# Performance work log

Hardware: AMD Instinct MI355X
Metric: run time of the kernel (lower is better)

The kernel has to match this reference:

```python
import jax, jax.numpy as jnp
import numpy as np

EPS = 1e-05
KEEP_RATIO = 0.7


def setup_inputs() -> dict:
    key = jax.random.key(0)
    ks = jax.random.split(key, 10)
    B, C, L, H = 8, 512, 8192, 128
    return {
        "x": jax.random.normal(ks[0], (B, C, L), dtype=jnp.float32),
        "c": jax.random.normal(ks[1], (B, C, L), dtype=jnp.float32),
        "gw1": jax.random.normal(ks[2], (H, C), dtype=jnp.float32) * 0.05,
        "gb1": jax.random.normal(ks[3], (H,), dtype=jnp.float32) * 0.05,
        "gw2": jax.random.normal(ks[4], (C, H), dtype=jnp.float32) * 0.05,
        "gb2": jax.random.normal(ks[5], (C,), dtype=jnp.float32) * 0.05,
        "mw1": jax.random.normal(ks[6], (H, C), dtype=jnp.float32) * 0.05,
        "mb1": jax.random.normal(ks[7], (H,), dtype=jnp.float32) * 0.05,
        "mw2": jax.random.normal(ks[8], (2 * C, H), dtype=jnp.float32) * 0.05,
        "mb2": jax.random.normal(ks[9], (2 * C,), dtype=jnp.float32) * 0.05,
    }


def reference(x, c, gw1, gb1, gw2, gb2, mw1, mb1, mw2, mb2):
    B, C, L = x.shape
    # per-channel stats over L
    mu_c = jnp.mean(x, axis=2, keepdims=True)                 # [B,C,1]
    var_c = jnp.var(x, axis=2, keepdims=True)                 # ddof=0
    sigma_c = jnp.sqrt(var_c + EPS)
    # per-sample stats over (C,L)
    mu_l = jnp.mean(x, axis=(1, 2), keepdims=True)            # [B,1,1]
    var_l = jnp.var(x, axis=(1, 2), keepdims=True)
    sigma_l = jnp.sqrt(var_l + EPS)
    # gate network on c (1x1 convs == channel matmuls), then mean over L
    h = jax.nn.relu(jnp.einsum('hc,bcl->bhl', gw1, c) + gb1[None, :, None])
    g = jax.nn.sigmoid(jnp.einsum('ch,bhl->bcl', gw2, h) + gb2[None, :, None])
    g_mix = jnp.mean(g, axis=2, keepdims=True)                # [B,C,1]
    mu = g_mix * mu_c + (1.0 - g_mix) * mu_l
    sigma = g_mix * sigma_c + (1.0 - g_mix) * sigma_l
    x_hat = (x - mu) / sigma
    # MLP on pooled condition -> gamma, beta
    cond_pool = jnp.mean(c, axis=2)                           # [B,C]
    hm = jax.nn.relu(jnp.einsum('hc,bc->bh', mw1, cond_pool) + mb1)
    gamma_beta = jnp.einsum('oh,bh->bo', mw2, hm) + mb2       # [B,2C]
    gamma = gamma_beta[:, :C][:, :, None]                     # [B,C,1]
    beta = gamma_beta[:, C:][:, :, None]
    y = (1.0 + gamma) * x_hat + beta
    # top-k channel mask by mean |y| over L
    imp = jnp.mean(jnp.abs(y), axis=2)                        # [B,C]
    k = max(1, int(C * KEEP_RATIO))
    _, idx = jax.lax.top_k(imp, k)                            # [B,k]
    mask = jnp.zeros((B, C), dtype=y.dtype).at[jnp.arange(B)[:, None], idx].set(1.0)
    return y * mask[:, :, None]
```

## Files before the change

kernel.cpp:

```cpp
#include <hip/hip_runtime.h>
#include <hip/hip_bf16.h>
#include <math.h>

#define NB 8
#define NC 512
#define NL 8192
#define NH 128
#define FEPS 1e-5f
#define NKEEP 358

typedef __attribute__((ext_vector_type(8))) short short8;
typedef __attribute__((ext_vector_type(4))) float f32x4;

__device__ __forceinline__ unsigned short f2bf(float x) {
  unsigned u = __float_as_uint(x);
  return (unsigned short)((u + 0x7fffu + ((u >> 16) & 1u)) >> 16);
}
__device__ __forceinline__ unsigned pack2(float a, float b) {
  return (unsigned)f2bf(a) | ((unsigned)f2bf(b) << 16);
}

__global__ __launch_bounds__(256) void k1_xstats(
    const float* __restrict__ x, float* __restrict__ xsum, float* __restrict__ xsumsq,
    const float* __restrict__ gw1, const float* __restrict__ gw2,
    unsigned short* __restrict__ gw1b, unsigned short* __restrict__ gw2b,
    float* __restrict__ csum, float* __restrict__ gsum) {
  const int bc = blockIdx.x;
  const int t = threadIdx.x;
  if (bc < 256) {
    const int i = bc * 256 + t;
    gw1b[i] = f2bf(gw1[i]);
    gw2b[i] = f2bf(gw2[i]);
    if (i < NB * NC) { csum[i] = 0.f; gsum[i] = 0.f; }
  }
  const float4* xp = reinterpret_cast<const float4*>(x + (size_t)bc * NL);
  float s1 = 0.f, s2 = 0.f;
#pragma unroll
  for (int i = 0; i < 8; ++i) {
    float4 v = xp[i * 256 + t];
    s1 += v.x + v.y + v.z + v.w;
    s2 += v.x * v.x + v.y * v.y + v.z * v.z + v.w * v.w;
  }
  for (int off = 32; off; off >>= 1) { s1 += __shfl_down(s1, off); s2 += __shfl_down(s2, off); }
  __shared__ float r1[4], r2[4];
  if ((t & 63) == 0) { r1[t >> 6] = s1; r2[t >> 6] = s2; }
  __syncthreads();
  if (t == 0) {
    xsum[bc]   = r1[0] + r1[1] + r1[2] + r1[3];
    xsumsq[bc] = r2[0] + r2[1] + r2[2] + r2[3];
  }
}

__global__ __launch_bounds__(256, 2) void k2_gate(
    const float* __restrict__ cin,
    const unsigned short* __restrict__ gw1b, const unsigned short* __restrict__ gw2b,
    const float* __restrict__ gb1, const float* __restrict__ gb2,
    float* __restrict__ gsum_g, float* __restrict__ csum_g) {
  __shared__ __align__(16) unsigned AsU[2 * 128 * 36];
  __shared__ __align__(16) unsigned short Hts[4][32][136];
  __shared__ float gsum_s[NC], csum_s[NC], gb2_s[NC];
  __shared__ float gb1_s[NH];

  const int t = threadIdx.x;
  const int lane = t & 63;
  const int w = t >> 6;
  const int r = lane & 15;
  const int kg = lane >> 4;
  const int b = blockIdx.x >> 6;
  const int l0 = (blockIdx.x & 63) * 128;

  const int p = t >> 3;
  const int q = t & 7;

  f32x4 acc0[8], acc1[8];
#pragma unroll
  for (int i = 0; i < 8; ++i) { acc0[i] = (f32x4){0.f,0.f,0.f,0.f}; acc1[i] = (f32x4){0.f,0.f,0.f,0.f}; }

  const float* cbase = cin + (size_t)b * NC * NL + l0;
  const unsigned short* gw1r = gw1b + (size_t)r * NC + kg * 8;

  f32x4 va[4], vb[4];

#define LOADA(kch) { \
    _Pragma("unroll") \
    for (int pass = 0; pass < 4; ++pass) { \
      const float* cp0 = cbase + (size_t)((kch) * 64 + 2 * p) * NL + 32 * pass + 4 * q; \
      va[pass] = __builtin_nontemporal_load(reinterpret_cast<const f32x4*>(cp0)); \
      vb[pass] = __builtin_nontemporal_load(reinterpret_cast<const f32x4*>(cp0 + NL)); \
    } }

#define WRITEA(kch, bufi) { \
    unsigned* dst = AsU + (bufi) * (128 * 36); \
    float sa = 0.f, sb = 0.f; \
    _Pragma("unroll") \
    for (int pass = 0; pass < 4; ++pass) { \
      const int ll = 32 * pass + 4 * q; \
      sa += va[pass].x + va[pass].y + va[pass].z + va[pass].w; \
      sb += vb[pass].x + vb[pass].y + vb[pass].z + vb[pass].w; \
      dst[(ll + 0) * 36 + p] = pack2(va[pass].x, vb[pass].x); \
      dst[(ll + 1) * 36 + p] = pack2(va[pass].y, vb[pass].y); \
      dst[(ll + 2) * 36 + p] = pack2(va[pass].z, vb[pass].z); \
      dst[(ll + 3) * 36 + p] = pack2(va[pass].w, vb[pass].w); \
    } \
    sa += __shfl_xor(sa, 1); sa += __shfl_xor(sa, 2); sa += __shfl_xor(sa, 4); \
    sb += __shfl_xor(sb, 1); sb += __shfl_xor(sb, 2); sb += __shfl_xor(sb, 4); \
    if ((lane & 7) == 0) { \
      atomicAdd(&csum_s[(kch) * 64 + 2 * p],     sa); \
      atomicAdd(&csum_s[(kch) * 64 + 2 * p + 1], sb); \
    } }

  LOADA(0)
  for (int i = t; i < NC; i += 256) { gsum_s[i] = 0.f; csum_s[i] = 0.f; gb2_s[i] = gb2[i]; }
  if (t < NH) gb1_s[t] = gb1[t];
  __syncthreads();
  WRITEA(0, 0)
  __syncthreads();

  for (int k = 0; k < 8; ++k) {
    const int cur = k & 1;
    if (k < 7) LOADA(k + 1)
    const unsigned* Abuf = AsU + cur * (128 * 36);
#pragma unroll
    for (int kk = 0; kk < 2; ++kk) {
      const short8 a0 = *reinterpret_cast<const short8*>(&Abuf[(32 * w + r)      * 36 + 16 * kk + 4 * kg]);
      const short8 a1 = *reinterpret_cast<const short8*>(&Abuf[(32 * w + 16 + r) * 36 + 16 * kk + 4 * kg]);
#pragma unroll
      for (int ht = 0; ht < 8; ++ht) {
        const short8 bf = *reinterpret_cast<const short8*>(
            gw1r + (size_t)(ht * 16) * NC + k * 64 + kk * 32);
        acc0[ht] = __builtin_amdgcn_mfma_f32_16x16x32_bf16(a0, bf, acc0[ht], 0, 0, 0);
        acc1[ht] = __builtin_amdgcn_mfma_f32_16x16x32_bf16(a1, bf, acc1[ht], 0, 0, 0);
      }
    }
    if (k < 7) WRITEA(k + 1, cur ^ 1)
    __syncthreads();
  }

#pragma unroll
  for (int ht = 0; ht < 8; ++ht) {
    const float bias = gb1_s[16 * ht + r];
#pragma unroll
    for (int reg = 0; reg < 4; ++reg) {
      Hts[w][4 * kg + reg][16 * ht + r]      = f2bf(fmaxf(acc0[ht][reg] + bias, 0.f));
      Hts[w][16 + 4 * kg + reg][16 * ht + r] = f2bf(fmaxf(acc1[ht][reg] + bias, 0.f));
    }
  }
  short8 af0[4], af1[4];
#pragma unroll
  for (int kk = 0; kk < 4; ++kk) {
    af0[kk] = *reinterpret_cast<const short8*>(&Hts[w][r][32 * kk + 8 * kg]);
    af1[kk] = *reinterpret_cast<const short8*>(&Hts[w][16 + r][32 * kk + 8 * kg]);
  }

  unsigned short* Bs2 = reinterpret_cast<unsigned short*>(AsU);
  const int crow = lane >> 4;
  const int bs2  = lane & 15;
  short8 bv[4];

#define LOADB2(ccn) { \
    _Pragma("unroll") \
    for (int j = 0; j < 4; ++j) { \
      const int cl = 16 * w + 4 * j + crow; \
      bv[j] = *reinterpret_cast<const short8*>(gw2b + (size_t)((ccn) * 64 + cl) * NH + bs2 * 8); \
    } }
#define WRITEB2(ccn) { \
    unsigned short* dstb = Bs2 + ((ccn) & 1) * 8192; \
    _Pragma("unroll") \
    for (int j = 0; j < 4; ++j) { \
      const int cl = 16 * w + 4 * j + crow; \
      *reinterpret_cast<short8*>(&dstb[cl * 128 + ((bs2 ^ (cl & 7)) * 8)]) = bv[j]; \
    } }

  LOADB2(0)
  WRITEB2(0)
  __syncthreads();
  for (int cc = 0; cc < 8; ++cc) {
    if (cc < 7) LOADB2(cc + 1)
    const unsigned short* Bbuf = Bs2 + (cc & 1) * 8192;
#pragma unroll
    for (int ctt = 0; ctt < 4; ++ctt) {
      f32x4 z0 = (f32x4){0.f,0.f,0.f,0.f}, z1 = (f32x4){0.f,0.f,0.f,0.f};
#pragma unroll
      for (int kk = 0; kk < 4; ++kk) {
        const short8 bf = *reinterpret_cast<const short8*>(
            &Bbuf[(16 * ctt + r) * 128 + (((4 * kk + kg) ^ (r & 7)) * 8)]);
        z0 = __builtin_amdgcn_mfma_f32_16x16x32_bf16(af0[kk], bf, z0, 0, 0, 0);
        z1 = __builtin_amdgcn_mfma_f32_16x16x32_bf16(af1[kk], bf, z1, 0, 0, 0);
      }
      const float bias = gb2_s[cc * 64 + 16 * ctt + r];
      float s = 0.f;
#pragma unroll
      for (int reg = 0; reg < 4; ++reg) {
        s += 1.f / (1.f + __expf(-(z0[reg] + bias)));
        s += 1.f / (1.f + __expf(-(z1[reg] + bias)));
      }
      s += __shfl_xor(s, 16);
      s += __shfl_xor(s, 32);
      if (lane < 16) atomicAdd(&gsum_s[cc * 64 + 16 * ctt + lane], s);
    }
    if (cc < 7) WRITEB2(cc + 1)
    __syncthreads();
  }
  for (int i = t; i < NC; i += 256) {
    atomicAdd(&gsum_g[b * NC + i], gsum_s[i]);
    atomicAdd(&csum_g[b * NC + i], csum_s[i]);
  }
}

__global__ __launch_bounds__(256) void k3_final(
    const float* __restrict__ xsum, const float* __restrict__ xsumsq,
    const float* __restrict__ csum, const float* __restrict__ gsum,
    const float* __restrict__ mw1, const float* __restrict__ mb1,
    const float* __restrict__ mw2, const float* __restrict__ mb2,
    float* __restrict__ a_arr, float* __restrict__ d_arr) {
  __shared__ __align__(16) float cp[NC];
  __shared__ __align__(16) float hm[NH];
  __shared__ float gbv[2 * NC];
  __shared__ double red[8];
  __shared__ float mu_l_s, sig_l_s;
  const int b = blockIdx.x, t = threadIdx.x;

  double s1 = 0.0, s2 = 0.0;
  for (int c = t; c < NC; c += 256) { s1 += (double)xsum[b * NC + c]; s2 += (double)xsumsq[b * NC + c]; }
  for (int off = 32; off; off >>= 1) { s1 += __shfl_down(s1, off); s2 += __shfl_down(s2, off); }
  if ((t & 63) == 0) { red[(t >> 6) * 2] = s1; red[(t >> 6) * 2 + 1] = s2; }
  for (int c = t; c < NC; c += 256) cp[c] = csum[b * NC + c] * (1.f / NL);
  __syncthreads();
  if (t == 0) {
    double S1 = red[0] + red[2] + red[4] + red[6];
    double S2 = red[1] + red[3] + red[5] + red[7];
    double n = (double)NC * NL;
    double mu = S1 / n;
    double var = S2 / n - mu * mu;
    mu_l_s = (float)mu;
    sig_l_s = (float)sqrt(var + (double)FEPS);
  }
  __syncthreads();
  if (t < NH) {
    const float4* row = reinterpret_cast<const float4*>(mw1 + (size_t)t * NC);
    const float4* cpv = reinterpret_cast<const float4*>(cp);
    float acc = mb1[t];
    for (int i = 0; i < NC / 4; ++i) {
      float4 wv = row[i], xv = cpv[i];
      acc += wv.x * xv.x + wv.y * xv.y + wv.z * xv.z + wv.w * xv.w;
    }
    hm[t] = fmaxf(acc, 0.f);
  }
  __syncthreads();
  for (int o = t; o < 2 * NC; o += 256) {
    const float4* row = reinterpret_cast<const float4*>(mw2 + (size_t)o * NH);
    const float4* hv = reinterpret_cast<const float4*>(hm);
    float acc = mb2[o];
    for (int i = 0; i < NH / 4; ++i) {
      float4 wv = row[i], xv = hv[i];
      acc += wv.x * xv.x + wv.y * xv.y + wv.z * xv.z + wv.w * xv.w;
    }
    gbv[o] = acc;
  }
  __syncthreads();
  const float mu_l = mu_l_s, sig_l = sig_l_s;
  for (int c = t; c < NC; c += 256) {
    float gm = gsum[b * NC + c] * (1.f / NL);
    double mu_c = (double)xsum[b * NC + c] / NL;
    double var_c = (double)xsumsq[b * NC + c] / NL - mu_c * mu_c;
    float sig_c = (float)sqrt(var_c + (double)FEPS);
    float mu = gm * (float)mu_c + (1.f - gm) * mu_l;
    float sg = gm * sig_c + (1.f - gm) * sig_l;
    float gamma = gbv[c], beta = gbv[NC + c];
    float A = (1.f + gamma) / sg;
    a_arr[b * NC + c] = A;
    d_arr[b * NC + c] = beta - A * mu;
  }
}

__global__ __launch_bounds__(256) void k4_y(
    const float* __restrict__ x, const float* __restrict__ a_arr,
    const float* __restrict__ d_arr, float* __restrict__ out, float* __restrict__ imp) {
  const int bc = blockIdx.x, t = threadIdx.x;
  const float A = a_arr[bc], D = d_arr[bc];
  const f32x4* xp = reinterpret_cast<const f32x4*>(x + (size_t)bc * NL);
  f32x4* op = reinterpret_cast<f32x4*>(out + (size_t)bc * NL);
  float s = 0.f;
#pragma unroll
  for (int i = 0; i < 8; ++i) {
    f32x4 v = __builtin_nontemporal_load(xp + i * 256 + t);
    f32x4 y;
    y.x = fmaf(A, v.x, D); y.y = fmaf(A, v.y, D);
    y.z = fmaf(A, v.z, D); y.w = fmaf(A, v.w, D);
    s += fabsf(y.x) + fabsf(y.y) + fabsf(y.z) + fabsf(y.w);
    __builtin_nontemporal_store(y, op + i * 256 + t);
  }
  for (int off = 32; off; off >>= 1) s += __shfl_down(s, off);
  __shared__ float rs[4];
  if ((t & 63) == 0) rs[t >> 6] = s;
  __syncthreads();
  if (t == 0) imp[bc] = rs[0] + rs[1] + rs[2] + rs[3];
}

__global__ __launch_bounds__(256) void k5_apply(
    const float* __restrict__ imp, float* __restrict__ out) {
  const int bc = blockIdx.x;
  const int b = bc >> 9;
  const int c = bc & (NC - 1);
  const int t = threadIdx.x;
  const float* row = imp + b * NC;
  const float mine = row[c];
  int cnt = 0;
#pragma unroll
  for (int jj = 0; jj < 2; ++jj) {
    const int j = jj * 256 + t;
    const float o = row[j];
    cnt += (o > mine) || (o == mine && j < c);
  }
  for (int off = 32; off; off >>= 1) cnt += __shfl_down(cnt, off);
  __shared__ int rs[4];
  if ((t & 63) == 0) rs[t >> 6] = cnt;
  __syncthreads();
  const int rank = rs[0] + rs[1] + rs[2] + rs[3];
  if (rank < NKEEP) return;
  f32x4* op = reinterpret_cast<f32x4*>(out + (size_t)bc * NL);
  const f32x4 z = (f32x4){0.f, 0.f, 0.f, 0.f};
#pragma unroll
  for (int i = 0; i < 8; ++i) __builtin_nontemporal_store(z, op + i * 256 + t);
}

extern "C" void kernel_launch(void* const* d_in, const int* in_sizes, int n_in,
                              void* d_out, int out_size, void* d_ws, size_t ws_size,
                              hipStream_t stream) {
  const float* x   = (const float*)d_in[0];
  const float* c   = (const float*)d_in[1];
  const float* gw1 = (const float*)d_in[2];
  const float* gb1 = (const float*)d_in[3];
  const float* gw2 = (const float*)d_in[4];
  const float* gb2 = (const float*)d_in[5];
  const float* mw1 = (const float*)d_in[6];
  const float* mb1 = (const float*)d_in[7];
  const float* mw2 = (const float*)d_in[8];
  const float* mb2 = (const float*)d_in[9];
  float* out = (float*)d_out;
  char* ws = (char*)d_ws;

  unsigned short* gw1b = (unsigned short*)(ws);
  unsigned short* gw2b = (unsigned short*)(ws + 131072);
  float* xsum   = (float*)(ws + 262144);
  float* xsumsq = (float*)(ws + 278528);
  float* csum   = (float*)(ws + 294912);
  float* gsum   = (float*)(ws + 311296);
  float* a_arr  = (float*)(ws + 327680);
  float* d_arr  = (float*)(ws + 344064);
  float* imp    = (float*)(ws + 360448);

  k1_xstats<<<NB * NC, 256, 0, stream>>>(x, xsum, xsumsq, gw1, gw2, gw1b, gw2b, csum, gsum);
  k2_gate<<<NB * (NL / 128), 256, 0, stream>>>(c, gw1b, gw2b, gb1, gb2, gsum, csum);
  k3_final<<<NB, 256, 0, stream>>>(xsum, xsumsq, csum, gsum, mw1, mb1, mw2, mb2, a_arr, d_arr);
  k4_y<<<NB * NC, 256, 0, stream>>>(x, a_arr, d_arr, out, imp);
  k5_apply<<<NB * NC, 256, 0, stream>>>(imp, out);
}
```

Baseline: 175.9 us.

## Fuse x statistics into gate kernel and double its block size to 512 threads

The per-channel sum and sum-of-squares reduction over x moves out of its own launch and into the gate GEMM kernel, where each wave streams one x row alongside the c tiles. Weight conversion and zeroing now run in a small separate prep kernel. The gate kernel goes from 256 to 512 threads, each wave owning 16 L-rows instead of 32, and per-channel c sums are written directly instead of through shared atomics. The aim is to overlap the x read with the c-side matrix work and drop a full-grid launch, at the cost of more memory traffic inside the gate kernel and more register and occupancy pressure.

```diff
diff --git a/kernel.cpp b/kernel.cpp
--- a/kernel.cpp
+++ b/kernel.cpp
@@ -20,44 +20,24 @@
   return (unsigned)f2bf(a) | ((unsigned)f2bf(b) << 16);
 }
 
-__global__ __launch_bounds__(256) void k1_xstats(
-    const float* __restrict__ x, float* __restrict__ xsum, float* __restrict__ xsumsq,
+__global__ __launch_bounds__(256) void k0_prep(
     const float* __restrict__ gw1, const float* __restrict__ gw2,
     unsigned short* __restrict__ gw1b, unsigned short* __restrict__ gw2b,
     float* __restrict__ csum, float* __restrict__ gsum) {
-  const int bc = blockIdx.x;
-  const int t = threadIdx.x;
-  if (bc < 256) {
-    const int i = bc * 256 + t;
-    gw1b[i] = f2bf(gw1[i]);
-    gw2b[i] = f2bf(gw2[i]);
-    if (i < NB * NC) { csum[i] = 0.f; gsum[i] = 0.f; }
-  }
-  const float4* xp = reinterpret_cast<const float4*>(x + (size_t)bc * NL);
-  float s1 = 0.f, s2 = 0.f;
-#pragma unroll
-  for (int i = 0; i < 8; ++i) {
-    float4 v = xp[i * 256 + t];
-    s1 += v.x + v.y + v.z + v.w;
-    s2 += v.x * v.x + v.y * v.y + v.z * v.z + v.w * v.w;
-  }
-  for (int off = 32; off; off >>= 1) { s1 += __shfl_down(s1, off); s2 += __shfl_down(s2, off); }
-  __shared__ float r1[4], r2[4];
-  if ((t & 63) == 0) { r1[t >> 6] = s1; r2[t >> 6] = s2; }
-  __syncthreads();
-  if (t == 0) {
-    xsum[bc]   = r1[0] + r1[1] + r1[2] + r1[3];
-    xsumsq[bc] = r2[0] + r2[1] + r2[2] + r2[3];
-  }
-}
-
-__global__ __launch_bounds__(256, 2) void k2_gate(
-    const float* __restrict__ cin,
+  int i = blockIdx.x * 256 + threadIdx.x;
+  gw1b[i] = f2bf(gw1[i]);
+  gw2b[i] = f2bf(gw2[i]);
+  if (i < NB * NC) { csum[i] = 0.f; gsum[i] = 0.f; }
+}
+
+__global__ __launch_bounds__(512, 4) void k2_gate(
+    const float* __restrict__ cin, const float* __restrict__ x,
     const unsigned short* __restrict__ gw1b, const unsigned short* __restrict__ gw2b,
     const float* __restrict__ gb1, const float* __restrict__ gb2,
-    float* __restrict__ gsum_g, float* __restrict__ csum_g) {
+    float* __restrict__ gsum_g, float* __restrict__ csum_g,
+    float* __restrict__ xsum, float* __restrict__ xsumsq) {
   __shared__ __align__(16) unsigned AsU[2 * 128 * 36];
-  __shared__ __align__(16) unsigned short Hts[4][32][136];
+  __shared__ __align__(16) unsigned short Hts[8][16][136];
   __shared__ float gsum_s[NC], csum_s[NC], gb2_s[NC];
   __shared__ float gb1_s[NH];
 
@@ -67,24 +47,28 @@
   const int r = lane & 15;
   const int kg = lane >> 4;
   const int b = blockIdx.x >> 6;
-  const int l0 = (blockIdx.x & 63) * 128;
-
-  const int p = t >> 3;
-  const int q = t & 7;
-
-  f32x4 acc0[8], acc1[8];
-#pragma unroll
-  for (int i = 0; i < 8; ++i) { acc0[i] = (f32x4){0.f,0.f,0.f,0.f}; acc1[i] = (f32x4){0.f,0.f,0.f,0.f}; }
+  const int lt = blockIdx.x & 63;
+  const int l0 = lt * 128;
+
+  const int p = t >> 4;
+  const int q = t & 15;
+
+  f32x4 acc[8];
+#pragma unroll
+  for (int i = 0; i < 8; ++i) acc[i] = (f32x4){0.f,0.f,0.f,0.f};
 
   const float* cbase = cin + (size_t)b * NC * NL + l0;
   const unsigned short* gw1r = gw1b + (size_t)r * NC + kg * 8;
 
-  f32x4 va[4], vb[4];
+  const f32x4* xp4 = reinterpret_cast<const f32x4*>(x + ((size_t)b * NC + lt * 8 + w) * NL);
+  float xs1 = 0.f, xs2 = 0.f;
+
+  f32x4 va[2], vb[2];
 
 #define LOADA(kch) { \
     _Pragma("unroll") \
-    for (int pass = 0; pass < 4; ++pass) { \
-      const float* cp0 = cbase + (size_t)((kch) * 64 + 2 * p) * NL + 32 * pass + 4 * q; \
+    for (int pass = 0; pass < 2; ++pass) { \
+      const float* cp0 = cbase + (size_t)((kch) * 64 + 2 * p) * NL + 64 * pass + 4 * q; \
       va[pass] = __builtin_nontemporal_load(reinterpret_cast<const f32x4*>(cp0)); \
       vb[pass] = __builtin_nontemporal_load(reinterpret_cast<const f32x4*>(cp0 + NL)); \
     } }
@@ -93,8 +77,8 @@
     unsigned* dst = AsU + (bufi) * (128 * 36); \
     float sa = 0.f, sb = 0.f; \
     _Pragma("unroll") \
-    for (int pass = 0; pass < 4; ++pass) { \
-      const int ll = 32 * pass + 4 * q; \
+    for (int pass = 0; pass < 2; ++pass) { \
+      const int ll = 64 * pass + 4 * q; \
       sa += va[pass].x + va[pass].y + va[pass].z + va[pass].w; \
       sb += vb[pass].x + vb[pass].y + vb[pass].z + vb[pass].w; \
       dst[(ll + 0) * 36 + p] = pack2(va[pass].x, vb[pass].x); \
@@ -102,15 +86,25 @@
       dst[(ll + 2) * 36 + p] = pack2(va[pass].z, vb[pass].z); \
       dst[(ll + 3) * 36 + p] = pack2(va[pass].w, vb[pass].w); \
     } \
-    sa += __shfl_xor(sa, 1); sa += __shfl_xor(sa, 2); sa += __shfl_xor(sa, 4); \
-    sb += __shfl_xor(sb, 1); sb += __shfl_xor(sb, 2); sb += __shfl_xor(sb, 4); \
-    if ((lane & 7) == 0) { \
-      atomicAdd(&csum_s[(kch) * 64 + 2 * p],     sa); \
-      atomicAdd(&csum_s[(kch) * 64 + 2 * p + 1], sb); \
+    sa += __shfl_xor(sa, 1); sa += __shfl_xor(sa, 2); \
+    sa += __shfl_xor(sa, 4); sa += __shfl_xor(sa, 8); \
+    sb += __shfl_xor(sb, 1); sb += __shfl_xor(sb, 2); \
+    sb += __shfl_xor(sb, 4); sb += __shfl_xor(sb, 8); \
+    if ((lane & 15) == 0) { \
+      csum_s[(kch) * 64 + 2 * p]     = sa; \
+      csum_s[(kch) * 64 + 2 * p + 1] = sb; \
+    } }
+
+#define XCHUNK(kch) { \
+    _Pragma("unroll") \
+    for (int j = 0; j < 4; ++j) { \
+      f32x4 v = xp4[lane + 64 * (4 * (kch) + j)]; \
+      xs1 += v.x + v.y + v.z + v.w; \
+      xs2 += v.x * v.x + v.y * v.y + v.z * v.z + v.w * v.w; \
     } }
 
   LOADA(0)
-  for (int i = t; i < NC; i += 256) { gsum_s[i] = 0.f; csum_s[i] = 0.f; gb2_s[i] = gb2[i]; }
+  for (int i = t; i < NC; i += 512) { gsum_s[i] = 0.f; gb2_s[i] = gb2[i]; }
   if (t < NH) gb1_s[t] = gb1[t];
   __syncthreads();
   WRITEA(0, 0)
@@ -119,55 +113,56 @@
   for (int k = 0; k < 8; ++k) {
     const int cur = k & 1;
     if (k < 7) LOADA(k + 1)
+    XCHUNK(k)
     const unsigned* Abuf = AsU + cur * (128 * 36);
 #pragma unroll
     for (int kk = 0; kk < 2; ++kk) {
-      const short8 a0 = *reinterpret_cast<const short8*>(&Abuf[(32 * w + r)      * 36 + 16 * kk + 4 * kg]);
-      const short8 a1 = *reinterpret_cast<const short8*>(&Abuf[(32 * w + 16 + r) * 36 + 16 * kk + 4 * kg]);
+      const short8 a = *reinterpret_cast<const short8*>(&Abuf[(16 * w + r) * 36 + 16 * kk + 4 * kg]);
 #pragma unroll
       for (int ht = 0; ht < 8; ++ht) {
         const short8 bf = *reinterpret_cast<const short8*>(
             gw1r + (size_t)(ht * 16) * NC + k * 64 + kk * 32);
-        acc0[ht] = __builtin_amdgcn_mfma_f32_16x16x32_bf16(a0, bf, acc0[ht], 0, 0, 0);
-        acc1[ht] = __builtin_amdgcn_mfma_f32_16x16x32_bf16(a1, bf, acc1[ht], 0, 0, 0);
+        acc[ht] = __builtin_amdgcn_mfma_f32_16x16x32_bf16(a, bf, acc[ht], 0, 0, 0);
       }
     }
     if (k < 7) WRITEA(k + 1, cur ^ 1)
     __syncthreads();
   }
 
+  for (int off = 32; off; off >>= 1) { xs1 += __shfl_down(xs1, off); xs2 += __shfl_down(xs2, off); }
+  if (lane == 0) {
+    xsum[b * NC + lt * 8 + w]   = xs1;
+    xsumsq[b * NC + lt * 8 + w] = xs2;
+  }
+
 #pragma unroll
   for (int ht = 0; ht < 8; ++ht) {
     const float bias = gb1_s[16 * ht + r];
 #pragma unroll
-    for (int reg = 0; reg < 4; ++reg) {
-      Hts[w][4 * kg + reg][16 * ht + r]      = f2bf(fmaxf(acc0[ht][reg] + bias, 0.f));
-      Hts[w][16 + 4 * kg + reg][16 * ht + r] = f2bf(fmaxf(acc1[ht][reg] + bias, 0.f));
-    }
-  }
-  short8 af0[4], af1[4];
-#pragma unroll
-  for (int kk = 0; kk < 4; ++kk) {
-    af0[kk] = *reinterpret_cast<const short8*>(&Hts[w][r][32 * kk + 8 * kg]);
-    af1[kk] = *reinterpret_cast<const short8*>(&Hts[w][16 + r][32 * kk + 8 * kg]);
-  }
+    for (int reg = 0; reg < 4; ++reg)
+      Hts[w][4 * kg + reg][16 * ht + r] = f2bf(fmaxf(acc[ht][reg] + bias, 0.f));
+  }
+  short8 af[4];
+#pragma unroll
+  for (int kk = 0; kk < 4; ++kk)
+    af[kk] = *reinterpret_cast<const short8*>(&Hts[w][r][32 * kk + 8 * kg]);
 
   unsigned short* Bs2 = reinterpret_cast<unsigned short*>(AsU);
   const int crow = lane >> 4;
   const int bs2  = lane & 15;
-  short8 bv[4];
+  short8 bv[2];
 
 #define LOADB2(ccn) { \
     _Pragma("unroll") \
-    for (int j = 0; j < 4; ++j) { \
-      const int cl = 16 * w + 4 * j + crow; \
+    for (int j = 0; j < 2; ++j) { \
+      const int cl = 8 * w + 4 * j + crow; \
       bv[j] = *reinterpret_cast<const short8*>(gw2b + (size_t)((ccn) * 64 + cl) * NH + bs2 * 8); \
     } }
 #define WRITEB2(ccn) { \
     unsigned short* dstb = Bs2 + ((ccn) & 1) * 8192; \
     _Pragma("unroll") \
-    for (int j = 0; j < 4; ++j) { \
-      const int cl = 16 * w + 4 * j + crow; \
+    for (int j = 0; j < 2; ++j) { \
+      const int cl = 8 * w + 4 * j + crow; \
       *reinterpret_cast<short8*>(&dstb[cl * 128 + ((bs2 ^ (cl & 7)) * 8)]) = bv[j]; \
     } }
 
@@ -179,21 +174,18 @@
     const unsigned short* Bbuf = Bs2 + (cc & 1) * 8192;
 #pragma unroll
     for (int ctt = 0; ctt < 4; ++ctt) {
-      f32x4 z0 = (f32x4){0.f,0.f,0.f,0.f}, z1 = (f32x4){0.f,0.f,0.f,0.f};
+      f32x4 z = (f32x4){0.f,0.f,0.f,0.f};
 #pragma unroll
       for (int kk = 0; kk < 4; ++kk) {
         const short8 bf = *reinterpret_cast<const short8*>(
             &Bbuf[(16 * ctt + r) * 128 + (((4 * kk + kg) ^ (r & 7)) * 8)]);
-        z0 = __builtin_amdgcn_mfma_f32_16x16x32_bf16(af0[kk], bf, z0, 0, 0, 0);
-        z1 = __builtin_amdgcn_mfma_f32_16x16x32_bf16(af1[kk], bf, z1, 0, 0, 0);
+        z = __builtin_amdgcn_mfma_f32_16x16x32_bf16(af[kk], bf, z, 0, 0, 0);
       }
       const float bias = gb2_s[cc * 64 + 16 * ctt + r];
       float s = 0.f;
 #pragma unroll
-      for (int reg = 0; reg < 4; ++reg) {
-        s += 1.f / (1.f + __expf(-(z0[reg] + bias)));
-        s += 1.f / (1.f + __expf(-(z1[reg] + bias)));
-      }
+      for (int reg = 0; reg < 4; ++reg)
+        s += 1.f / (1.f + __expf(-(z[reg] + bias)));
       s += __shfl_xor(s, 16);
       s += __shfl_xor(s, 32);
       if (lane < 16) atomicAdd(&gsum_s[cc * 64 + 16 * ctt + lane], s);
@@ -201,7 +193,7 @@
     if (cc < 7) WRITEB2(cc + 1)
     __syncthreads();
   }
-  for (int i = t; i < NC; i += 256) {
+  for (int i = t; i < NC; i += 512) {
     atomicAdd(&gsum_g[b * NC + i], gsum_s[i]);
     atomicAdd(&csum_g[b * NC + i], csum_s[i]);
   }
@@ -350,8 +342,8 @@
   float* d_arr  = (float*)(ws + 344064);
   float* imp    = (float*)(ws + 360448);
 
-  k1_xstats<<<NB * NC, 256, 0, stream>>>(x, xsum, xsumsq, gw1, gw2, gw1b, gw2b, csum, gsum);
-  k2_gate<<<NB * (NL / 128), 256, 0, stream>>>(c, gw1b, gw2b, gb1, gb2, gsum, csum);
+  k0_prep<<<256, 256, 0, stream>>>(gw1, gw2, gw1b, gw2b, csum, gsum);
+  k2_gate<<<NB * (NL / 128), 512, 0, stream>>>(c, x, gw1b, gw2b, gb1, gb2, gsum, csum, xsum, xsumsq);
   k3_final<<<NB, 256, 0, stream>>>(xsum, xsumsq, csum, gsum, mw1, mb1, mw2, mb2, a_arr, d_arr);
   k4_y<<<NB * NC, 256, 0, stream>>>(x, a_arr, d_arr, out, imp);
   k5_apply<<<NB * NC, 256, 0, stream>>>(imp, out);
```

After: 195.1 us. 1.11x slower.

## Halve gate-kernel L tile, raise occupancy, read gw2 fragments directly from global

Applied to the files above, without the earlier changes.

The gate kernel now processes 64 positions per block instead of 128, doubling the grid and halving accumulators, LDS and register use so four blocks can fit per CU. The gw2 LDS double-buffer staging and its per-chunk barriers are removed, and B fragments are loaded straight from global/L2. gw1 fragments are prefetched into registers before the A-tile loads, with sched barriers to control ordering. Per-block weight traffic roughly doubles because each block reloads gw1/gw2 for half the work, and global atomics also double.

```diff
diff --git a/kernel.cpp b/kernel.cpp
--- a/kernel.cpp
+++ b/kernel.cpp
@@ -51,13 +51,12 @@
   }
 }
 
-__global__ __launch_bounds__(256, 2) void k2_gate(
+__global__ __launch_bounds__(256, 4) void k2_gate(
     const float* __restrict__ cin,
     const unsigned short* __restrict__ gw1b, const unsigned short* __restrict__ gw2b,
     const float* __restrict__ gb1, const float* __restrict__ gb2,
     float* __restrict__ gsum_g, float* __restrict__ csum_g) {
-  __shared__ __align__(16) unsigned AsU[2 * 128 * 36];
-  __shared__ __align__(16) unsigned short Hts[4][32][136];
+  __shared__ __align__(16) unsigned AsU[2 * 64 * 36];
   __shared__ float gsum_s[NC], csum_s[NC], gb2_s[NC];
   __shared__ float gb1_s[NH];
 
@@ -66,34 +65,34 @@
   const int w = t >> 6;
   const int r = lane & 15;
   const int kg = lane >> 4;
-  const int b = blockIdx.x >> 6;
-  const int l0 = (blockIdx.x & 63) * 128;
+  const int b = blockIdx.x >> 7;
+  const int l0 = (blockIdx.x & 127) * 64;
 
   const int p = t >> 3;
   const int q = t & 7;
 
-  f32x4 acc0[8], acc1[8];
-#pragma unroll
-  for (int i = 0; i < 8; ++i) { acc0[i] = (f32x4){0.f,0.f,0.f,0.f}; acc1[i] = (f32x4){0.f,0.f,0.f,0.f}; }
+  f32x4 acc[8];
+#pragma unroll
+  for (int i = 0; i < 8; ++i) acc[i] = (f32x4){0.f,0.f,0.f,0.f};
 
   const float* cbase = cin + (size_t)b * NC * NL + l0;
   const unsigned short* gw1r = gw1b + (size_t)r * NC + kg * 8;
 
-  f32x4 va[4], vb[4];
+  f32x4 va[2], vb[2];
 
 #define LOADA(kch) { \
     _Pragma("unroll") \
-    for (int pass = 0; pass < 4; ++pass) { \
+    for (int pass = 0; pass < 2; ++pass) { \
       const float* cp0 = cbase + (size_t)((kch) * 64 + 2 * p) * NL + 32 * pass + 4 * q; \
       va[pass] = __builtin_nontemporal_load(reinterpret_cast<const f32x4*>(cp0)); \
       vb[pass] = __builtin_nontemporal_load(reinterpret_cast<const f32x4*>(cp0 + NL)); \
     } }
 
 #define WRITEA(kch, bufi) { \
-    unsigned* dst = AsU + (bufi) * (128 * 36); \
+    unsigned* dst = AsU + (bufi) * (64 * 36); \
     float sa = 0.f, sb = 0.f; \
     _Pragma("unroll") \
-    for (int pass = 0; pass < 4; ++pass) { \
+    for (int pass = 0; pass < 2; ++pass) { \
       const int ll = 32 * pass + 4 * q; \
       sa += va[pass].x + va[pass].y + va[pass].z + va[pass].w; \
       sb += vb[pass].x + vb[pass].y + vb[pass].z + vb[pass].w; \
@@ -105,102 +104,74 @@
     sa += __shfl_xor(sa, 1); sa += __shfl_xor(sa, 2); sa += __shfl_xor(sa, 4); \
     sb += __shfl_xor(sb, 1); sb += __shfl_xor(sb, 2); sb += __shfl_xor(sb, 4); \
     if ((lane & 7) == 0) { \
-      atomicAdd(&csum_s[(kch) * 64 + 2 * p],     sa); \
-      atomicAdd(&csum_s[(kch) * 64 + 2 * p + 1], sb); \
+      csum_s[(kch) * 64 + 2 * p]     = sa; \
+      csum_s[(kch) * 64 + 2 * p + 1] = sb; \
     } }
 
   LOADA(0)
-  for (int i = t; i < NC; i += 256) { gsum_s[i] = 0.f; csum_s[i] = 0.f; gb2_s[i] = gb2[i]; }
+  for (int i = t; i < NC; i += 256) { gsum_s[i] = 0.f; gb2_s[i] = gb2[i]; }
   if (t < NH) gb1_s[t] = gb1[t];
   __syncthreads();
   WRITEA(0, 0)
   __syncthreads();
 
   for (int k = 0; k < 8; ++k) {
-    const int cur = k & 1;
+    short8 bfr[16];
+#pragma unroll
+    for (int ht = 0; ht < 8; ++ht) {
+      bfr[2 * ht]     = *reinterpret_cast<const short8*>(gw1r + (size_t)(ht * 16) * NC + k * 64);
+      bfr[2 * ht + 1] = *reinterpret_cast<const short8*>(gw1r + (size_t)(ht * 16) * NC + k * 64 + 32);
+    }
+    __builtin_amdgcn_sched_barrier(0);
     if (k < 7) LOADA(k + 1)
-    const unsigned* Abuf = AsU + cur * (128 * 36);
+    __builtin_amdgcn_sched_barrier(0);
+    const unsigned* Abuf = AsU + (k & 1) * (64 * 36);
 #pragma unroll
     for (int kk = 0; kk < 2; ++kk) {
-      const short8 a0 = *reinterpret_cast<const short8*>(&Abuf[(32 * w + r)      * 36 + 16 * kk + 4 * kg]);
-      const short8 a1 = *reinterpret_cast<const short8*>(&Abuf[(32 * w + 16 + r) * 36 + 16 * kk + 4 * kg]);
-#pragma unroll
-      for (int ht = 0; ht < 8; ++ht) {
-        const short8 bf = *reinterpret_cast<const short8*>(
-            gw1r + (size_t)(ht * 16) * NC + k * 64 + kk * 32);
-        acc0[ht] = __builtin_amdgcn_mfma_f32_16x16x32_bf16(a0, bf, acc0[ht], 0, 0, 0);
-        acc1[ht] = __builtin_amdgcn_mfma_f32_16x16x32_bf16(a1, bf, acc1[ht], 0, 0, 0);
-      }
-    }
-    if (k < 7) WRITEA(k + 1, cur ^ 1)
+      const short8 a = *reinterpret_cast<const short8*>(&Abuf[(16 * w + r) * 36 + 16 * kk + 4 * kg]);
+#pragma unroll
+      for (int ht = 0; ht < 8; ++ht)
+        acc[ht] = __builtin_amdgcn_mfma_f32_16x16x32_bf16(a, bfr[2 * ht + kk], acc[ht], 0, 0, 0);
+    }
+    if (k < 7) WRITEA(k + 1, (k + 1) & 1)
     __syncthreads();
   }
 
+  unsigned short (*Hts)[16][136] = reinterpret_cast<unsigned short (*)[16][136]>(AsU);
 #pragma unroll
   for (int ht = 0; ht < 8; ++ht) {
     const float bias = gb1_s[16 * ht + r];
 #pragma unroll
-    for (int reg = 0; reg < 4; ++reg) {
-      Hts[w][4 * kg + reg][16 * ht + r]      = f2bf(fmaxf(acc0[ht][reg] + bias, 0.f));
-      Hts[w][16 + 4 * kg + reg][16 * ht + r] = f2bf(fmaxf(acc1[ht][reg] + bias, 0.f));
-    }
-  }
-  short8 af0[4], af1[4];
-#pragma unroll
-  for (int kk = 0; kk < 4; ++kk) {
-    af0[kk] = *reinterpret_cast<const short8*>(&Hts[w][r][32 * kk + 8 * kg]);
-    af1[kk] = *reinterpret_cast<const short8*>(&Hts[w][16 + r][32 * kk + 8 * kg]);
-  }
-
-  unsigned short* Bs2 = reinterpret_cast<unsigned short*>(AsU);
-  const int crow = lane >> 4;
-  const int bs2  = lane & 15;
-  short8 bv[4];
-
-#define LOADB2(ccn) { \
-    _Pragma("unroll") \
-    for (int j = 0; j < 4; ++j) { \
-      const int cl = 16 * w + 4 * j + crow; \
-      bv[j] = *reinterpret_cast<const short8*>(gw2b + (size_t)((ccn) * 64 + cl) * NH + bs2 * 8); \
-    } }
-#define WRITEB2(ccn) { \
-    unsigned short* dstb = Bs2 + ((ccn) & 1) * 8192; \
-    _Pragma("unroll") \
-    for (int j = 0; j < 4; ++j) { \
-      const int cl = 16 * w + 4 * j + crow; \
-      *reinterpret_cast<short8*>(&dstb[cl * 128 + ((bs2 ^ (cl & 7)) * 8)]) = bv[j]; \
-    } }
-
-  LOADB2(0)
-  WRITEB2(0)
-  __syncthreads();
+    for (int reg = 0; reg < 4; ++reg)
+      Hts[w][4 * kg + reg][16 * ht + r] = f2bf(fmaxf(acc[ht][reg] + bias, 0.f));
+  }
+  short8 af[4];
+#pragma unroll
+  for (int kk = 0; kk < 4; ++kk)
+    af[kk] = *reinterpret_cast<const short8*>(&Hts[w][r][32 * kk + 8 * kg]);
+
+  const unsigned short* gw2r = gw2b + (size_t)r * NH + kg * 8;
   for (int cc = 0; cc < 8; ++cc) {
-    if (cc < 7) LOADB2(cc + 1)
-    const unsigned short* Bbuf = Bs2 + (cc & 1) * 8192;
 #pragma unroll
     for (int ctt = 0; ctt < 4; ++ctt) {
-      f32x4 z0 = (f32x4){0.f,0.f,0.f,0.f}, z1 = (f32x4){0.f,0.f,0.f,0.f};
+      f32x4 z = (f32x4){0.f,0.f,0.f,0.f};
 #pragma unroll
       for (int kk = 0; kk < 4; ++kk) {
         const short8 bf = *reinterpret_cast<const short8*>(
-            &Bbuf[(16 * ctt + r) * 128 + (((4 * kk + kg) ^ (r & 7)) * 8)]);
-        z0 = __builtin_amdgcn_mfma_f32_16x16x32_bf16(af0[kk], bf, z0, 0, 0, 0);
-        z1 = __builtin_amdgcn_mfma_f32_16x16x32_bf16(af1[kk], bf, z1, 0, 0, 0);
+            gw2r + (size_t)(cc * 64 + 16 * ctt) * NH + kk * 32);
+        z = __builtin_amdgcn_mfma_f32_16x16x32_bf16(af[kk], bf, z, 0, 0, 0);
       }
       const float bias = gb2_s[cc * 64 + 16 * ctt + r];
       float s = 0.f;
 #pragma unroll
-      for (int reg = 0; reg < 4; ++reg) {
-        s += 1.f / (1.f + __expf(-(z0[reg] + bias)));
-        s += 1.f / (1.f + __expf(-(z1[reg] + bias)));
-      }
+      for (int reg = 0; reg < 4; ++reg)
+        s += 1.f / (1.f + __expf(-(z[reg] + bias)));
       s += __shfl_xor(s, 16);
       s += __shfl_xor(s, 32);
       if (lane < 16) atomicAdd(&gsum_s[cc * 64 + 16 * ctt + lane], s);
     }
-    if (cc < 7) WRITEB2(cc + 1)
-    __syncthreads();
-  }
+  }
+  __syncthreads();
   for (int i = t; i < NC; i += 256) {
     atomicAdd(&gsum_g[b * NC + i], gsum_s[i]);
     atomicAdd(&csum_g[b * NC + i], csum_s[i]);
@@ -351,7 +322,7 @@
   float* imp    = (float*)(ws + 360448);
 
   k1_xstats<<<NB * NC, 256, 0, stream>>>(x, xsum, xsumsq, gw1, gw2, gw1b, gw2b, csum, gsum);
-  k2_gate<<<NB * (NL / 128), 256, 0, stream>>>(c, gw1b, gw2b, gb1, gb2, gsum, csum);
+  k2_gate<<<NB * (NL / 64), 256, 0, stream>>>(c, gw1b, gw2b, gb1, gb2, gsum, csum);
   k3_final<<<NB, 256, 0, stream>>>(xsum, xsumsq, csum, gsum, mw1, mb1, mw2, mb2, a_arr, d_arr);
   k4_y<<<NB * NC, 256, 0, stream>>>(x, a_arr, d_arr, out, imp);
   k5_apply<<<NB * NC, 256, 0, stream>>>(imp, out);
```

Measured after the change: 234.4 us. 33.3% more time.

## Fuse per-channel x statistics into the gate GEMM kernel

Applied to the files above, without the earlier changes.

The standalone x-statistics pass is removed and folded into the gate kernel. Each of the 512 gate blocks now also streams 8 rows of x and reduces their sum and sum of squares, interleaving those loads with the GEMM main loop. A small prep kernel keeps the weight conversion and zeroing. The aim is to overlap the memory-bound x read with the compute-bound gate GEMM and save a launch, at the cost of more register pressure and memory traffic inside the gate kernel.

```diff
diff --git a/kernel.cpp b/kernel.cpp
--- a/kernel.cpp
+++ b/kernel.cpp
@@ -20,42 +20,22 @@
   return (unsigned)f2bf(a) | ((unsigned)f2bf(b) << 16);
 }
 
-__global__ __launch_bounds__(256) void k1_xstats(
-    const float* __restrict__ x, float* __restrict__ xsum, float* __restrict__ xsumsq,
+__global__ __launch_bounds__(256) void k0_prep(
     const float* __restrict__ gw1, const float* __restrict__ gw2,
     unsigned short* __restrict__ gw1b, unsigned short* __restrict__ gw2b,
     float* __restrict__ csum, float* __restrict__ gsum) {
-  const int bc = blockIdx.x;
-  const int t = threadIdx.x;
-  if (bc < 256) {
-    const int i = bc * 256 + t;
-    gw1b[i] = f2bf(gw1[i]);
-    gw2b[i] = f2bf(gw2[i]);
-    if (i < NB * NC) { csum[i] = 0.f; gsum[i] = 0.f; }
-  }
-  const float4* xp = reinterpret_cast<const float4*>(x + (size_t)bc * NL);
-  float s1 = 0.f, s2 = 0.f;
-#pragma unroll
-  for (int i = 0; i < 8; ++i) {
-    float4 v = xp[i * 256 + t];
-    s1 += v.x + v.y + v.z + v.w;
-    s2 += v.x * v.x + v.y * v.y + v.z * v.z + v.w * v.w;
-  }
-  for (int off = 32; off; off >>= 1) { s1 += __shfl_down(s1, off); s2 += __shfl_down(s2, off); }
-  __shared__ float r1[4], r2[4];
-  if ((t & 63) == 0) { r1[t >> 6] = s1; r2[t >> 6] = s2; }
-  __syncthreads();
-  if (t == 0) {
-    xsum[bc]   = r1[0] + r1[1] + r1[2] + r1[3];
-    xsumsq[bc] = r2[0] + r2[1] + r2[2] + r2[3];
-  }
+  int i = blockIdx.x * 256 + threadIdx.x;
+  gw1b[i] = f2bf(gw1[i]);
+  gw2b[i] = f2bf(gw2[i]);
+  if (i < NB * NC) { csum[i] = 0.f; gsum[i] = 0.f; }
 }
 
 __global__ __launch_bounds__(256, 2) void k2_gate(
-    const float* __restrict__ cin,
+    const float* __restrict__ cin, const float* __restrict__ x,
     const unsigned short* __restrict__ gw1b, const unsigned short* __restrict__ gw2b,
     const float* __restrict__ gb1, const float* __restrict__ gb2,
-    float* __restrict__ gsum_g, float* __restrict__ csum_g) {
+    float* __restrict__ gsum_g, float* __restrict__ csum_g,
+    float* __restrict__ xsum, float* __restrict__ xsumsq) {
   __shared__ __align__(16) unsigned AsU[2 * 128 * 36];
   __shared__ __align__(16) unsigned short Hts[4][32][136];
   __shared__ float gsum_s[NC], csum_s[NC], gb2_s[NC];
@@ -78,6 +58,12 @@
 
   const float* cbase = cin + (size_t)b * NC * NL + l0;
   const unsigned short* gw1r = gw1b + (size_t)r * NC + kg * 8;
+
+  const int xr = t >> 5;
+  const int xq = t & 31;
+  const float* xrow = x + ((size_t)blockIdx.x * 8 + xr) * NL + 4 * xq;
+  f32x4 xv[8];
+  float xs1 = 0.f, xs2 = 0.f;
 
   f32x4 va[4], vb[4];
 
@@ -109,6 +95,19 @@
       atomicAdd(&csum_s[(kch) * 64 + 2 * p + 1], sb); \
     } }
 
+#define XLOAD(kch) { \
+    _Pragma("unroll") \
+    for (int i = 0; i < 8; ++i) \
+      xv[i] = *reinterpret_cast<const f32x4*>(xrow + (kch) * 1024 + 128 * i); }
+
+#define XACC() { \
+    _Pragma("unroll") \
+    for (int i = 0; i < 8; ++i) { \
+      f32x4 v_ = xv[i]; \
+      xs1 += v_.x + v_.y + v_.z + v_.w; \
+      xs2 += v_.x * v_.x + v_.y * v_.y + v_.z * v_.z + v_.w * v_.w; \
+    } }
+
   LOADA(0)
   for (int i = t; i < NC; i += 256) { gsum_s[i] = 0.f; csum_s[i] = 0.f; gb2_s[i] = gb2[i]; }
   if (t < NH) gb1_s[t] = gb1[t];
@@ -118,6 +117,7 @@
 
   for (int k = 0; k < 8; ++k) {
     const int cur = k & 1;
+    XLOAD(k)
     if (k < 7) LOADA(k + 1)
     const unsigned* Abuf = AsU + cur * (128 * 36);
 #pragma unroll
@@ -133,7 +133,14 @@
       }
     }
     if (k < 7) WRITEA(k + 1, cur ^ 1)
+    XACC()
     __syncthreads();
+  }
+
+  for (int off = 16; off; off >>= 1) { xs1 += __shfl_down(xs1, off); xs2 += __shfl_down(xs2, off); }
+  if (xq == 0) {
+    xsum[blockIdx.x * 8 + xr]   = xs1;
+    xsumsq[blockIdx.x * 8 + xr] = xs2;
   }
 
 #pragma unroll
@@ -350,8 +357,8 @@
   float* d_arr  = (float*)(ws + 344064);
   float* imp    = (float*)(ws + 360448);
 
-  k1_xstats<<<NB * NC, 256, 0, stream>>>(x, xsum, xsumsq, gw1, gw2, gw1b, gw2b, csum, gsum);
-  k2_gate<<<NB * (NL / 128), 256, 0, stream>>>(c, gw1b, gw2b, gb1, gb2, gsum, csum);
+  k0_prep<<<256, 256, 0, stream>>>(gw1, gw2, gw1b, gw2b, csum, gsum);
+  k2_gate<<<NB * (NL / 128), 256, 0, stream>>>(c, x, gw1b, gw2b, gb1, gb2, gsum, csum, xsum, xsumsq);
   k3_final<<<NB, 256, 0, stream>>>(xsum, xsumsq, csum, gsum, mw1, mb1, mw2, mb2, a_arr, d_arr);
   k4_y<<<NB * NC, 256, 0, stream>>>(x, a_arr, d_arr, out, imp);
   k5_apply<<<NB * NC, 256, 0, stream>>>(imp, out);
```

Result: slower. 182.3 us (+3.7%).
